# Kernel tuning notes

Hardware: AMD Instinct MI355X
Metric: run time of the kernel (lower is better)

The kernel has to match this reference:

```python
import jax, jax.numpy as jnp
import numpy as np

IMG_W = 256; IMG_H = 256; N_PTS = 320
MIN_DEPTH = 3.0; MAX_DEPTH = 9.0; NDC_EXTENT = 1.0
SCALING = 0.1; EA_EPS = 1e-10; NORM_EPS = 1e-8


def setup_inputs() -> dict:
    key = jax.random.key(0)
    B, D = 1, 256
    image3d = jax.random.uniform(key, (B, 1, D, D, D), dtype=jnp.float32)
    # PyTorch3D convention: X_cam = X_world @ R + T. Camera at z=-6 world looking at origin.
    R = jnp.tile(jnp.eye(3, dtype=jnp.float32)[None], (B, 1, 1))
    T = jnp.tile(jnp.array([[0.0, 0.0, 6.0]], dtype=jnp.float32), (B, 1))
    focal = jnp.full((B,), 1.7320508, dtype=jnp.float32)  # NDC focal, fov ~ 60deg
    return {"image3d": image3d, "R": R, "T": T, "focal": focal}


def _trilinear_sample(vol, pts):
    # vol: [C, D, H, W]; pts: [N, 3] in xyz order, normalized coords in [-1, 1]
    # (grid_sample semantics: align_corners=True, padding_mode='zeros')
    C, D, H, W = vol.shape
    sizes = jnp.array([W, H, D], dtype=pts.dtype)
    idx = (pts + 1.0) * 0.5 * (sizes - 1.0)
    i0f = jnp.floor(idx)
    frac = idx - i0f
    i0 = i0f.astype(jnp.int32)
    volf = vol.reshape(C, -1)
    out = jnp.zeros((C, pts.shape[0]), dtype=vol.dtype)
    for dz in (0, 1):
        for dy in (0, 1):
            for dx in (0, 1):
                ix = i0[:, 0] + dx; iy = i0[:, 1] + dy; iz = i0[:, 2] + dz
                w = ((frac[:, 0] if dx else 1.0 - frac[:, 0]) *
                     (frac[:, 1] if dy else 1.0 - frac[:, 1]) *
                     (frac[:, 2] if dz else 1.0 - frac[:, 2]))
                valid = (ix >= 0) & (ix < W) & (iy >= 0) & (iy < H) & (iz >= 0) & (iz < D)
                lin = (jnp.clip(iz, 0, D - 1) * H + jnp.clip(iy, 0, H - 1)) * W + jnp.clip(ix, 0, W - 1)
                out = out + jnp.where(valid, w, 0.0)[None, :] * volf[:, lin]
    return out


def reference(image3d, R, T, focal):
    B, Cin, D, H, W = image3d.shape
    # features = image3d.repeat(1,3,1,1,1) when single channel
    features = jnp.broadcast_to(image3d, (B, 3, D, H, W)) if Cin == 1 else image3d
    densities = jnp.ones_like(image3d[:, :1]) * SCALING  # [B,1,D,H,W]
    shape = max(Cin, D)
    voxel_size = 2.0 * NDC_EXTENT / shape
    # Volumes local coords: world extent voxel_size*(size-1) maps to [-1,1]
    half_extent = jnp.array([voxel_size * (W - 1) / 2.0,
                             voxel_size * (H - 1) / 2.0,
                             voxel_size * (D - 1) / 2.0], dtype=image3d.dtype)
    # NDC pixel-center grid (PyTorch3D: +x left, +y up)
    xs = jnp.linspace(1.0 - 1.0 / IMG_W, -(1.0 - 1.0 / IMG_W), IMG_W, dtype=image3d.dtype)
    ys = jnp.linspace(1.0 - 1.0 / IMG_H, -(1.0 - 1.0 / IMG_H), IMG_H, dtype=image3d.dtype)
    depths = jnp.linspace(MIN_DEPTH, MAX_DEPTH, N_PTS, dtype=image3d.dtype)
    gy, gx = jnp.meshgrid(ys, xs, indexing="ij")  # [Hi, Wi]
    f = focal[:, None, None, None]
    dd = depths[None, None, None, :]
    x_cam = gx[None, :, :, None] * dd / f
    y_cam = gy[None, :, :, None] * dd / f
    z_cam = jnp.broadcast_to(dd, x_cam.shape)
    pts_cam = jnp.stack([x_cam, y_cam, z_cam], axis=-1)  # [B, Hi, Wi, P, 3]
    # unproject: X_world = (X_cam - T) @ R^T, i.e. X_world_i = sum_j (Xc - T)_j R_ij
    pts_world = jnp.einsum('bhwpj,bij->bhwpi', pts_cam - T[:, None, None, None, :], R)
    pts_local = pts_world / half_extent
    vol = jnp.concatenate([features, densities], axis=1)  # [B, 4, D, H, W]
    N = IMG_H * IMG_W * N_PTS
    vals = jax.vmap(_trilinear_sample)(vol, pts_local.reshape(B, N, 3))  # [B, 4, N]
    vals = vals.reshape(B, 4, IMG_H, IMG_W, N_PTS)
    feats = vals[:, :3]           # [B, 3, Hi, Wi, P]
    dens = vals[:, 3]             # [B, Hi, Wi, P]
    # EmissionAbsorption raymarcher: shifted cumprod absorption, alpha compositing
    cp = jnp.cumprod((1.0 + EA_EPS) - dens, axis=-1)
    absorption = jnp.concatenate([jnp.ones_like(cp[..., :1]), cp[..., :-1]], axis=-1)
    weights = dens * absorption
    rgb = jnp.einsum('bhwp,bchwp->bhwc', weights, feats)      # [B, Hi, Wi, 3]
    opacity = 1.0 - jnp.prod(1.0 - dens, axis=-1)             # [B, Hi, Wi]
    rgba = jnp.concatenate([rgb, opacity[..., None]], axis=-1)  # [B, Hi, Wi, 4]
    screen = jnp.transpose(rgba, (0, 3, 2, 1))                # [B, 4, Wi, Hi]
    gray = screen.mean(axis=1, keepdims=True)                 # is_grayscale=True
    return (gray + NORM_EPS) / (gray.max() + NORM_EPS)        # minimized()
```

## Files before the change

kernel.cpp:

```cpp
#include <hip/hip_runtime.h>

#define IMG_W 256
#define IMG_H 256
#define N_PTS 320
#define VD 256
#define VH 256
#define VW 256
#define PX 8
#define NC 32
#define DSTEP (6.0f / (N_PTS - 1))

__global__ __launch_bounds__(256) void render_kernel(
    const float* __restrict__ vol,
    const float* __restrict__ Rm,
    const float* __restrict__ Tv,
    const float* __restrict__ focal,
    float* __restrict__ out,
    unsigned int* __restrict__ maxbits)
{
    const int tx = threadIdx.x;
    const int ty = threadIdx.y;
    const int w  = blockIdx.x * PX + tx;
    const int h  = blockIdx.y;

    const float a  = 1.0f - 1.0f / IMG_W;
    const float gx = a - (2.0f * a / (IMG_W - 1)) * (float)w;
    const float gy = a - (2.0f * a / (IMG_H - 1)) * (float)h;

    const float f  = focal[0];
    const float ux = gx / f, uy = gy / f;

    const float R00 = Rm[0], R01 = Rm[1], R02 = Rm[2];
    const float R10 = Rm[3], R11 = Rm[4], R12 = Rm[5];
    const float R20 = Rm[6], R21 = Rm[7], R22 = Rm[8];
    const float Tx = Tv[0], Ty = Tv[1], Tz = Tv[2];

    const float Bx = R00 * ux + R01 * uy + R02;
    const float By = R10 * ux + R11 * uy + R12;
    const float Bz = R20 * ux + R21 * uy + R22;
    const float Ax = -(R00 * Tx + R01 * Ty + R02 * Tz);
    const float Ay = -(R10 * Tx + R11 * Ty + R12 * Tz);
    const float Az = -(R20 * Tx + R21 * Ty + R22 * Tz);

    const float voxel = 2.0f / 256.0f;
    const float hx = voxel * (VW - 1) * 0.5f;
    const float hy = voxel * (VH - 1) * 0.5f;
    const float hz = voxel * (VD - 1) * 0.5f;

    const float sxc = 0.5f * (VW - 1) / hx, oxc = 0.5f * (VW - 1);
    const float syc = 0.5f * (VH - 1) / hy, oyc = 0.5f * (VH - 1);
    const float szc = 0.5f * (VD - 1) / hz, ozc = 0.5f * (VD - 1);
    const float fBx = Bx * sxc, fAx = Ax * sxc + oxc;
    const float fBy = By * syc, fAy = Ay * syc + oyc;
    const float fBz = Bz * szc, fAz = Az * szc + ozc;

    float dlo = 3.0f, dhi = 9.0f;
    {
        const float lo = -1.0f, hi = 256.0f;
        #pragma unroll
        for (int dim = 0; dim < 3; ++dim) {
            const float fA = dim == 0 ? fAx : (dim == 1 ? fAy : fAz);
            const float fB = dim == 0 ? fBx : (dim == 1 ? fBy : fBz);
            if (fabsf(fB) > 1e-12f) {
                const float r = 1.0f / fB;
                const float t0 = (lo - fA) * r, t1 = (hi - fA) * r;
                dlo = fmaxf(dlo, fminf(t0, t1));
                dhi = fminf(dhi, fmaxf(t0, t1));
            } else if (fA < lo || fA >= hi) {
                dhi = -1.0f;
            }
        }
    }
    int pmin = 0, pmax = 0;
    if (dhi > dlo) {
        pmin = max(0, (int)floorf((dlo - 3.0f) / DSTEP) - 1);
        pmax = min(N_PTS, (int)ceilf((dhi - 3.0f) / DSTEP) + 2);
        if (pmax < pmin) pmax = pmin;
    }

    const int len = pmax - pmin;
    const int plo = pmin + ((len * ty) >> 5);
    const int phi = pmin + ((len * (ty + 1)) >> 5);

    float S = 0.0f;
    float A = 1.0f;

    #pragma unroll 2
    for (int p = plo; p < phi; ++p) {
        const float d = 3.0f + (float)p * DSTEP;

        const float fx = fmaf(fBx, d, fAx);
        const float fy = fmaf(fBy, d, fAy);
        const float fz = fmaf(fBz, d, fAz);

        const float flx = floorf(fx), fly = floorf(fy), flz = floorf(fz);
        const int ix0 = (int)flx, iy0 = (int)fly, iz0 = (int)flz;

        float dens = 0.0f, feat = 0.0f;
        if (ix0 >= -1 && ix0 < VW && iy0 >= -1 && iy0 < VH && iz0 >= -1 && iz0 < VD) {
            const float frx = fx - flx, fry = fy - fly, frz = fz - flz;
            float wx0 = 1.0f - frx, wx1 = frx;
            float wy0 = 1.0f - fry, wy1 = fry;
            float wz0 = 1.0f - frz, wz1 = frz;
            if (ix0 < 0)       wx0 = 0.0f;
            if (ix0 + 1 >= VW) wx1 = 0.0f;
            if (iy0 < 0)       wy0 = 0.0f;
            if (iy0 + 1 >= VH) wy1 = 0.0f;
            if (iz0 < 0)       wz0 = 0.0f;
            if (iz0 + 1 >= VD) wz1 = 0.0f;

            const int cx0 = max(ix0, 0), cx1 = min(ix0 + 1, VW - 1);
            const int cy0 = max(iy0, 0), cy1 = min(iy0 + 1, VH - 1);
            const int cz0 = max(iz0, 0), cz1 = min(iz0 + 1, VD - 1);

            const int zb0 = cz0 * (VH * VW), zb1 = cz1 * (VH * VW);
            const int yb0 = cy0 * VW,        yb1 = cy1 * VW;

            const float v000 = vol[zb0 + yb0 + cx0];
            const float v001 = vol[zb0 + yb0 + cx1];
            const float v010 = vol[zb0 + yb1 + cx0];
            const float v011 = vol[zb0 + yb1 + cx1];
            const float v100 = vol[zb1 + yb0 + cx0];
            const float v101 = vol[zb1 + yb0 + cx1];
            const float v110 = vol[zb1 + yb1 + cx0];
            const float v111 = vol[zb1 + yb1 + cx1];

            const float w00 = wy0 * wz0, w01 = wy1 * wz0;
            const float w10 = wy0 * wz1, w11 = wy1 * wz1;
            const float c000 = wx0 * w00, c001 = wx1 * w00;
            const float c010 = wx0 * w01, c011 = wx1 * w01;
            const float c100 = wx0 * w10, c101 = wx1 * w10;
            const float c110 = wx0 * w11, c111 = wx1 * w11;

            feat = c000 * v000 + c001 * v001 + c010 * v010 + c011 * v011
                 + c100 * v100 + c101 * v101 + c110 * v110 + c111 * v111;
            dens = 0.1f * (c000 + c001 + c010 + c011 + c100 + c101 + c110 + c111);
        }

        S = fmaf(dens * A, feat, S);
        A *= (1.0f - dens);
    }

    __shared__ float lS[NC][PX];
    __shared__ float lA[NC][PX];
    lS[ty][tx] = S;
    lA[ty][tx] = A;
    __syncthreads();

    if (ty == 0) {
        float Stot = 0.0f, Atot = 1.0f;
        #pragma unroll
        for (int c = 0; c < NC; ++c) {
            Stot = fmaf(Atot, lS[c][tx], Stot);
            Atot *= lA[c][tx];
        }
        const float gray = (3.0f * Stot + (1.0f - Atot)) * 0.25f;
        out[w * IMG_H + h] = gray;

        float m = gray;
        m = fmaxf(m, __shfl_down(m, 4));
        m = fmaxf(m, __shfl_down(m, 2));
        m = fmaxf(m, __shfl_down(m, 1));
        if (tx == 0 && m > 0.0f)
            atomicMax(maxbits, __float_as_uint(m));
    }
}

__global__ __launch_bounds__(256) void normalize_kernel(
    float* __restrict__ out, const unsigned int* __restrict__ maxbits)
{
    const int i = blockIdx.x * blockDim.x + threadIdx.x;
    const float m = __uint_as_float(*maxbits);
    out[i] = (out[i] + 1e-8f) / (m + 1e-8f);
}

extern "C" void kernel_launch(void* const* d_in, const int* in_sizes, int n_in,
                              void* d_out, int out_size, void* d_ws, size_t ws_size,
                              hipStream_t stream) {
    (void)in_sizes; (void)n_in; (void)out_size; (void)ws_size;
    const float* vol   = (const float*)d_in[0];
    const float* Rm    = (const float*)d_in[1];
    const float* Tv    = (const float*)d_in[2];
    const float* focal = (const float*)d_in[3];
    float* out = (float*)d_out;
    unsigned int* maxbits = (unsigned int*)d_ws;

    hipMemsetAsync(d_ws, 0, 4, stream);

    dim3 block(PX, NC, 1);
    dim3 grid(IMG_W / PX, IMG_H, 1);
    render_kernel<<<grid, block, 0, stream>>>(vol, Rm, Tv, focal, out, maxbits);

    normalize_kernel<<<(IMG_W * IMG_H) / 256, 256, 0, stream>>>(out, maxbits);
}
```

Before: 115.1 us.

## Compact active rays into a work list before rendering

Adds a prep kernel that computes each ray's clipped sample range, writes zero for rays that miss the volume, and compacts the active rays into a workspace list using wave ballot and an atomic counter. The render kernel then processes only listed rays, 16 rays per block with 16 chunks each, so blocks for empty rays exit early. This adds a kernel launch and some extra global traffic, and the atomic append makes the ray order nondeterministic, which can hurt spatial locality of volume reads.

```diff
diff --git a/kernel.cpp b/kernel.cpp
--- a/kernel.cpp
+++ b/kernel.cpp
@@ -6,92 +6,134 @@
 #define VD 256
 #define VH 256
 #define VW 256
-#define PX 8
-#define NC 32
 #define DSTEP (6.0f / (N_PTS - 1))
-
-__global__ __launch_bounds__(256) void render_kernel(
-    const float* __restrict__ vol,
-    const float* __restrict__ Rm,
-    const float* __restrict__ Tv,
-    const float* __restrict__ focal,
-    float* __restrict__ out,
-    unsigned int* __restrict__ maxbits)
-{
-    const int tx = threadIdx.x;
-    const int ty = threadIdx.y;
-    const int w  = blockIdx.x * PX + tx;
-    const int h  = blockIdx.y;
-
+#define RPB 16
+#define CPR 16
+
+
+struct RayCoef { float fAx, fBx, fAy, fBy, fAz, fBz; };
+
+__device__ __forceinline__ RayCoef ray_coef(int w, int h,
+                                            const float* __restrict__ Rm,
+                                            const float* __restrict__ Tv,
+                                            const float* __restrict__ focal) {
     const float a  = 1.0f - 1.0f / IMG_W;
     const float gx = a - (2.0f * a / (IMG_W - 1)) * (float)w;
     const float gy = a - (2.0f * a / (IMG_H - 1)) * (float)h;
-
     const float f  = focal[0];
     const float ux = gx / f, uy = gy / f;
-
     const float R00 = Rm[0], R01 = Rm[1], R02 = Rm[2];
     const float R10 = Rm[3], R11 = Rm[4], R12 = Rm[5];
     const float R20 = Rm[6], R21 = Rm[7], R22 = Rm[8];
     const float Tx = Tv[0], Ty = Tv[1], Tz = Tv[2];
-
     const float Bx = R00 * ux + R01 * uy + R02;
     const float By = R10 * ux + R11 * uy + R12;
     const float Bz = R20 * ux + R21 * uy + R22;
     const float Ax = -(R00 * Tx + R01 * Ty + R02 * Tz);
     const float Ay = -(R10 * Tx + R11 * Ty + R12 * Tz);
     const float Az = -(R20 * Tx + R21 * Ty + R22 * Tz);
-
     const float voxel = 2.0f / 256.0f;
     const float hx = voxel * (VW - 1) * 0.5f;
     const float hy = voxel * (VH - 1) * 0.5f;
     const float hz = voxel * (VD - 1) * 0.5f;
-
     const float sxc = 0.5f * (VW - 1) / hx, oxc = 0.5f * (VW - 1);
     const float syc = 0.5f * (VH - 1) / hy, oyc = 0.5f * (VH - 1);
     const float szc = 0.5f * (VD - 1) / hz, ozc = 0.5f * (VD - 1);
-    const float fBx = Bx * sxc, fAx = Ax * sxc + oxc;
-    const float fBy = By * syc, fAy = Ay * syc + oyc;
-    const float fBz = Bz * szc, fAz = Az * szc + ozc;
-
+    RayCoef rc;
+    rc.fBx = Bx * sxc; rc.fAx = Ax * sxc + oxc;
+    rc.fBy = By * syc; rc.fAy = Ay * syc + oyc;
+    rc.fBz = Bz * szc; rc.fAz = Az * szc + ozc;
+    return rc;
+}
+
+__device__ __forceinline__ void clip_ray(const RayCoef& rc, int& pmin, int& len) {
     float dlo = 3.0f, dhi = 9.0f;
-    {
-        const float lo = -1.0f, hi = 256.0f;
-        #pragma unroll
-        for (int dim = 0; dim < 3; ++dim) {
-            const float fA = dim == 0 ? fAx : (dim == 1 ? fAy : fAz);
-            const float fB = dim == 0 ? fBx : (dim == 1 ? fBy : fBz);
-            if (fabsf(fB) > 1e-12f) {
-                const float r = 1.0f / fB;
-                const float t0 = (lo - fA) * r, t1 = (hi - fA) * r;
-                dlo = fmaxf(dlo, fminf(t0, t1));
-                dhi = fminf(dhi, fmaxf(t0, t1));
-            } else if (fA < lo || fA >= hi) {
-                dhi = -1.0f;
-            }
-        }
-    }
-    int pmin = 0, pmax = 0;
+    const float lo = -1.0f, hi = 256.0f;
+    const float fA[3] = { rc.fAx, rc.fAy, rc.fAz };
+    const float fB[3] = { rc.fBx, rc.fBy, rc.fBz };
+    #pragma unroll
+    for (int dim = 0; dim < 3; ++dim) {
+        if (fabsf(fB[dim]) > 1e-12f) {
+            const float r = 1.0f / fB[dim];
+            const float t0 = (lo - fA[dim]) * r, t1 = (hi - fA[dim]) * r;
+            dlo = fmaxf(dlo, fminf(t0, t1));
+            dhi = fminf(dhi, fmaxf(t0, t1));
+        } else if (fA[dim] < lo || fA[dim] >= hi) {
+            dhi = -1.0f;
+        }
+    }
+    pmin = 0; len = 0;
     if (dhi > dlo) {
         pmin = max(0, (int)floorf((dlo - 3.0f) / DSTEP) - 1);
-        pmax = min(N_PTS, (int)ceilf((dhi - 3.0f) / DSTEP) + 2);
-        if (pmax < pmin) pmax = pmin;
-    }
-
-    const int len = pmax - pmin;
-    const int plo = pmin + ((len * ty) >> 5);
-    const int phi = pmin + ((len * (ty + 1)) >> 5);
-
-    float S = 0.0f;
-    float A = 1.0f;
-
-    #pragma unroll 2
+        int pmax = min(N_PTS, (int)ceilf((dhi - 3.0f) / DSTEP) + 2);
+        len = max(0, pmax - pmin);
+    }
+}
+
+__global__ __launch_bounds__(256) void prep_kernel(
+    const float* __restrict__ Rm, const float* __restrict__ Tv,
+    const float* __restrict__ focal, float* __restrict__ out,
+    unsigned int* __restrict__ wsu)
+{
+    const int w = threadIdx.x;
+    const int h = blockIdx.x;
+    const RayCoef rc = ray_coef(w, h, Rm, Tv, focal);
+    int pmin, len;
+    clip_ray(rc, pmin, len);
+
+    const bool active = (len > 0);
+    if (!active) out[w * IMG_H + h] = 0.0f;
+
+    const unsigned long long mask = __ballot(active);
+    const int lane = threadIdx.x & 63;
+    const int cnt  = __popcll(mask);
+    if (cnt) {
+        const int leader = __ffsll(mask) - 1;
+        unsigned int base = 0;
+        if (lane == leader) base = atomicAdd(&wsu[1], (unsigned)cnt);
+        base = __shfl(base, leader);
+        if (active) {
+            const int rank = __popcll(mask & ((1ull << lane) - 1ull));
+            uint2 e;
+            e.x = (unsigned)(h * IMG_W + w) | ((unsigned)pmin << 16);
+            e.y = (unsigned)len;
+            ((uint2*)(wsu + 2))[base + rank] = e;
+        }
+    }
+}
+
+__global__ __launch_bounds__(256) void render_kernel(
+    const float* __restrict__ vol, const float* __restrict__ Rm,
+    const float* __restrict__ Tv, const float* __restrict__ focal,
+    float* __restrict__ out, unsigned int* __restrict__ wsu)
+{
+    const unsigned count = wsu[1];
+    if (blockIdx.x * RPB >= count) return;
+
+    const int tx = threadIdx.x;
+    const int ty = threadIdx.y;
+    const unsigned slot = blockIdx.x * RPB + tx;
+    const bool valid = (slot < count);
+
+    uint2 e = make_uint2(0u, 0u);
+    if (valid) e = ((const uint2*)(wsu + 2))[slot];
+    const int rayid = (int)(e.x & 0xffffu);
+    const int pmin  = (int)(e.x >> 16);
+    const int len   = (int)e.y;
+    const int w = rayid & (IMG_W - 1);
+    const int h = rayid >> 8;
+
+    const RayCoef rc = ray_coef(w, h, Rm, Tv, focal);
+
+    const int plo = pmin + ((len * ty) >> 4);
+    const int phi = pmin + ((len * (ty + 1)) >> 4);
+
+    float S = 0.0f, A = 1.0f;
     for (int p = plo; p < phi; ++p) {
         const float d = 3.0f + (float)p * DSTEP;
-
-        const float fx = fmaf(fBx, d, fAx);
-        const float fy = fmaf(fBy, d, fAy);
-        const float fz = fmaf(fBz, d, fAz);
+        const float fx = fmaf(rc.fBx, d, rc.fAx);
+        const float fy = fmaf(rc.fBy, d, rc.fAy);
+        const float fz = fmaf(rc.fBz, d, rc.fAz);
 
         const float flx = floorf(fx), fly = floorf(fy), flz = floorf(fz);
         const int ix0 = (int)flx, iy0 = (int)fly, iz0 = (int)flz;
@@ -141,8 +183,8 @@
         A *= (1.0f - dens);
     }
 
-    __shared__ float lS[NC][PX];
-    __shared__ float lA[NC][PX];
+    __shared__ float lS[CPR][RPB];
+    __shared__ float lA[CPR][RPB];
     lS[ty][tx] = S;
     lA[ty][tx] = A;
     __syncthreads();
@@ -150,27 +192,28 @@
     if (ty == 0) {
         float Stot = 0.0f, Atot = 1.0f;
         #pragma unroll
-        for (int c = 0; c < NC; ++c) {
+        for (int c = 0; c < CPR; ++c) {
             Stot = fmaf(Atot, lS[c][tx], Stot);
             Atot *= lA[c][tx];
         }
         const float gray = (3.0f * Stot + (1.0f - Atot)) * 0.25f;
-        out[w * IMG_H + h] = gray;
-
-        float m = gray;
+        if (valid) out[w * IMG_H + h] = gray;
+
+        float m = valid ? gray : 0.0f;
+        m = fmaxf(m, __shfl_down(m, 8));
         m = fmaxf(m, __shfl_down(m, 4));
         m = fmaxf(m, __shfl_down(m, 2));
         m = fmaxf(m, __shfl_down(m, 1));
         if (tx == 0 && m > 0.0f)
-            atomicMax(maxbits, __float_as_uint(m));
+            atomicMax(&wsu[0], __float_as_uint(m));
     }
 }
 
 __global__ __launch_bounds__(256) void normalize_kernel(
-    float* __restrict__ out, const unsigned int* __restrict__ maxbits)
+    float* __restrict__ out, const unsigned int* __restrict__ wsu)
 {
     const int i = blockIdx.x * blockDim.x + threadIdx.x;
-    const float m = __uint_as_float(*maxbits);
+    const float m = __uint_as_float(wsu[0]);
     out[i] = (out[i] + 1e-8f) / (m + 1e-8f);
 }
 
@@ -183,13 +226,15 @@
     const float* Tv    = (const float*)d_in[2];
     const float* focal = (const float*)d_in[3];
     float* out = (float*)d_out;
-    unsigned int* maxbits = (unsigned int*)d_ws;
-
-    hipMemsetAsync(d_ws, 0, 4, stream);
-
-    dim3 block(PX, NC, 1);
-    dim3 grid(IMG_W / PX, IMG_H, 1);
-    render_kernel<<<grid, block, 0, stream>>>(vol, Rm, Tv, focal, out, maxbits);
-
-    normalize_kernel<<<(IMG_W * IMG_H) / 256, 256, 0, stream>>>(out, maxbits);
-}
+    unsigned int* wsu = (unsigned int*)d_ws;
+
+    hipMemsetAsync(d_ws, 0, 8, stream);
+
+    prep_kernel<<<IMG_H, IMG_W, 0, stream>>>(Rm, Tv, focal, out, wsu);
+
+    dim3 rblock(RPB, CPR, 1);
+    dim3 rgrid((IMG_W * IMG_H + RPB - 1) / RPB, 1, 1);
+    render_kernel<<<rgrid, rblock, 0, stream>>>(vol, Rm, Tv, focal, out, wsu);
+
+    normalize_kernel<<<(IMG_W * IMG_H) / 256, 256, 0, stream>>>(out, wsu);
+}
```

New measurement: 108.0 us. 1.07x faster.

## Drop memset and atomics, fuse max-reduce and normalize into one-block kernel

Applied to the files above, without the earlier changes.

Removes the hipMemsetAsync and the per-block atomicMax, replacing them with a single 1024-thread kernel that loads the whole 64K-pixel image into registers, reduces the max, and writes the normalized values. It also reshapes the render block from 8 pixels x 32 ray chunks to 16 pixels x 16 chunks, which gives longer per-thread marching segments and a wider pixel row per wave. It drops the unroll-2 pragma as well. The aim is to cut launch and atomic overhead; the cost is a single-block normalize pass that cannot use the whole GPU and shorter parallel splitting along each ray.

```diff
diff --git a/kernel.cpp b/kernel.cpp
--- a/kernel.cpp
+++ b/kernel.cpp
@@ -6,50 +6,43 @@
 #define VD 256
 #define VH 256
 #define VW 256
-#define PX 8
-#define NC 32
 #define DSTEP (6.0f / (N_PTS - 1))
+#define TPX 16
+#define CPR 16
 
 __global__ __launch_bounds__(256) void render_kernel(
     const float* __restrict__ vol,
-    const float* __restrict__ Rm,
-    const float* __restrict__ Tv,
+    const float* __restrict__ Rm, const float* __restrict__ Tv,
     const float* __restrict__ focal,
-    float* __restrict__ out,
-    unsigned int* __restrict__ maxbits)
+    float* __restrict__ out)
 {
     const int tx = threadIdx.x;
     const int ty = threadIdx.y;
-    const int w  = blockIdx.x * PX + tx;
+    const int w  = blockIdx.x * TPX + tx;
     const int h  = blockIdx.y;
 
     const float a  = 1.0f - 1.0f / IMG_W;
     const float gx = a - (2.0f * a / (IMG_W - 1)) * (float)w;
     const float gy = a - (2.0f * a / (IMG_H - 1)) * (float)h;
-
     const float f  = focal[0];
     const float ux = gx / f, uy = gy / f;
-
     const float R00 = Rm[0], R01 = Rm[1], R02 = Rm[2];
     const float R10 = Rm[3], R11 = Rm[4], R12 = Rm[5];
     const float R20 = Rm[6], R21 = Rm[7], R22 = Rm[8];
     const float Tx = Tv[0], Ty = Tv[1], Tz = Tv[2];
-
     const float Bx = R00 * ux + R01 * uy + R02;
     const float By = R10 * ux + R11 * uy + R12;
     const float Bz = R20 * ux + R21 * uy + R22;
     const float Ax = -(R00 * Tx + R01 * Ty + R02 * Tz);
     const float Ay = -(R10 * Tx + R11 * Ty + R12 * Tz);
     const float Az = -(R20 * Tx + R21 * Ty + R22 * Tz);
-
     const float voxel = 2.0f / 256.0f;
-    const float hx = voxel * (VW - 1) * 0.5f;
-    const float hy = voxel * (VH - 1) * 0.5f;
-    const float hz = voxel * (VD - 1) * 0.5f;
-
-    const float sxc = 0.5f * (VW - 1) / hx, oxc = 0.5f * (VW - 1);
-    const float syc = 0.5f * (VH - 1) / hy, oyc = 0.5f * (VH - 1);
-    const float szc = 0.5f * (VD - 1) / hz, ozc = 0.5f * (VD - 1);
+    const float hxe = voxel * (VW - 1) * 0.5f;
+    const float hye = voxel * (VH - 1) * 0.5f;
+    const float hze = voxel * (VD - 1) * 0.5f;
+    const float sxc = 0.5f * (VW - 1) / hxe, oxc = 0.5f * (VW - 1);
+    const float syc = 0.5f * (VH - 1) / hye, oyc = 0.5f * (VH - 1);
+    const float szc = 0.5f * (VD - 1) / hze, ozc = 0.5f * (VD - 1);
     const float fBx = Bx * sxc, fAx = Ax * sxc + oxc;
     const float fBy = By * syc, fAy = Ay * syc + oyc;
     const float fBz = Bz * szc, fAz = Az * szc + ozc;
@@ -57,38 +50,33 @@
     float dlo = 3.0f, dhi = 9.0f;
     {
         const float lo = -1.0f, hi = 256.0f;
+        const float fA[3] = { fAx, fAy, fAz };
+        const float fB[3] = { fBx, fBy, fBz };
         #pragma unroll
         for (int dim = 0; dim < 3; ++dim) {
-            const float fA = dim == 0 ? fAx : (dim == 1 ? fAy : fAz);
-            const float fB = dim == 0 ? fBx : (dim == 1 ? fBy : fBz);
-            if (fabsf(fB) > 1e-12f) {
-                const float r = 1.0f / fB;
-                const float t0 = (lo - fA) * r, t1 = (hi - fA) * r;
+            if (fabsf(fB[dim]) > 1e-12f) {
+                const float r = 1.0f / fB[dim];
+                const float t0 = (lo - fA[dim]) * r, t1 = (hi - fA[dim]) * r;
                 dlo = fmaxf(dlo, fminf(t0, t1));
                 dhi = fminf(dhi, fmaxf(t0, t1));
-            } else if (fA < lo || fA >= hi) {
+            } else if (fA[dim] < lo || fA[dim] >= hi) {
                 dhi = -1.0f;
             }
         }
     }
-    int pmin = 0, pmax = 0;
+    int pmin = 0, len = 0;
     if (dhi > dlo) {
         pmin = max(0, (int)floorf((dlo - 3.0f) / DSTEP) - 1);
-        pmax = min(N_PTS, (int)ceilf((dhi - 3.0f) / DSTEP) + 2);
-        if (pmax < pmin) pmax = pmin;
-    }
-
-    const int len = pmax - pmin;
-    const int plo = pmin + ((len * ty) >> 5);
-    const int phi = pmin + ((len * (ty + 1)) >> 5);
-
-    float S = 0.0f;
-    float A = 1.0f;
-
-    #pragma unroll 2
+        const int pmax = min(N_PTS, (int)ceilf((dhi - 3.0f) / DSTEP) + 2);
+        len = max(0, pmax - pmin);
+    }
+
+    const int plo = pmin + ((len * ty) >> 4);
+    const int phi = pmin + ((len * (ty + 1)) >> 4);
+
+    float S = 0.0f, A = 1.0f;
     for (int p = plo; p < phi; ++p) {
         const float d = 3.0f + (float)p * DSTEP;
-
         const float fx = fmaf(fBx, d, fAx);
         const float fy = fmaf(fBy, d, fAy);
         const float fz = fmaf(fBz, d, fAz);
@@ -141,8 +129,8 @@
         A *= (1.0f - dens);
     }
 
-    __shared__ float lS[NC][PX];
-    __shared__ float lA[NC][PX];
+    __shared__ float lS[CPR][TPX];
+    __shared__ float lA[CPR][TPX];
     lS[ty][tx] = S;
     lA[ty][tx] = A;
     __syncthreads();
@@ -150,46 +138,70 @@
     if (ty == 0) {
         float Stot = 0.0f, Atot = 1.0f;
         #pragma unroll
-        for (int c = 0; c < NC; ++c) {
+        for (int c = 0; c < CPR; ++c) {
             Stot = fmaf(Atot, lS[c][tx], Stot);
             Atot *= lA[c][tx];
         }
         const float gray = (3.0f * Stot + (1.0f - Atot)) * 0.25f;
         out[w * IMG_H + h] = gray;
-
-        float m = gray;
-        m = fmaxf(m, __shfl_down(m, 4));
-        m = fmaxf(m, __shfl_down(m, 2));
-        m = fmaxf(m, __shfl_down(m, 1));
-        if (tx == 0 && m > 0.0f)
-            atomicMax(maxbits, __float_as_uint(m));
     }
 }
 
-__global__ __launch_bounds__(256) void normalize_kernel(
-    float* __restrict__ out, const unsigned int* __restrict__ maxbits)
+__global__ __launch_bounds__(1024) void maxnorm_kernel(float* __restrict__ out)
 {
-    const int i = blockIdx.x * blockDim.x + threadIdx.x;
-    const float m = __uint_as_float(*maxbits);
-    out[i] = (out[i] + 1e-8f) / (m + 1e-8f);
+    float4* o4 = (float4*)out;
+    const int tid = threadIdx.x;
+    const int NV4 = (IMG_W * IMG_H) / 4;
+
+    float4 v[16];
+    float m = 0.0f;
+    #pragma unroll
+    for (int k = 0; k < 16; ++k) {
+        v[k] = o4[tid + k * 1024];
+        m = fmaxf(m, fmaxf(fmaxf(v[k].x, v[k].y), fmaxf(v[k].z, v[k].w)));
+    }
+
+    #pragma unroll
+    for (int off = 32; off > 0; off >>= 1)
+        m = fmaxf(m, __shfl_down(m, off));
+
+    __shared__ float lm[16];
+    if ((tid & 63) == 0) lm[tid >> 6] = m;
+    __syncthreads();
+    if (tid == 0) {
+        float mm = lm[0];
+        #pragma unroll
+        for (int i = 1; i < 16; ++i) mm = fmaxf(mm, lm[i]);
+        lm[0] = mm;
+    }
+    __syncthreads();
+    const float inv = 1.0f / (lm[0] + 1e-8f);
+
+    #pragma unroll
+    for (int k = 0; k < 16; ++k) {
+        float4 r;
+        r.x = (v[k].x + 1e-8f) * inv;
+        r.y = (v[k].y + 1e-8f) * inv;
+        r.z = (v[k].z + 1e-8f) * inv;
+        r.w = (v[k].w + 1e-8f) * inv;
+        o4[tid + k * 1024] = r;
+    }
+    (void)NV4;
 }
 
 extern "C" void kernel_launch(void* const* d_in, const int* in_sizes, int n_in,
                               void* d_out, int out_size, void* d_ws, size_t ws_size,
                               hipStream_t stream) {
-    (void)in_sizes; (void)n_in; (void)out_size; (void)ws_size;
+    (void)in_sizes; (void)n_in; (void)out_size; (void)d_ws; (void)ws_size;
     const float* vol   = (const float*)d_in[0];
     const float* Rm    = (const float*)d_in[1];
     const float* Tv    = (const float*)d_in[2];
     const float* focal = (const float*)d_in[3];
     float* out = (float*)d_out;
-    unsigned int* maxbits = (unsigned int*)d_ws;
-
-    hipMemsetAsync(d_ws, 0, 4, stream);
-
-    dim3 block(PX, NC, 1);
-    dim3 grid(IMG_W / PX, IMG_H, 1);
-    render_kernel<<<grid, block, 0, stream>>>(vol, Rm, Tv, focal, out, maxbits);
-
-    normalize_kernel<<<(IMG_W * IMG_H) / 256, 256, 0, stream>>>(out, maxbits);
+
+    dim3 rblock(TPX, CPR, 1);
+    dim3 rgrid(IMG_W / TPX, IMG_H, 1);
+    render_kernel<<<rgrid, rblock, 0, stream>>>(vol, Rm, Tv, focal, out);
+
+    maxnorm_kernel<<<1, 1024, 0, stream>>>(out);
 }
```

New measurement: 112.6 us. -2.2%, faster.
